# Optimization experiments

Measured on AMD Instinct MI355X. Metric: run time of the kernel, lower is better.

## Reference

```python
import jax, jax.numpy as jnp
import numpy as np

SEGMENT_LENGTHS = [1024, 2048, 4096]
DILATION_RATES = [1, 2, 4]


def _head_groups(num_heads, num_segments):
    base = num_heads // num_segments
    extra = num_heads % num_segments
    groups = [base] * num_segments
    for i in range(extra):
        groups[-(i + 1)] += 1
    return groups


def _dilated_indices(segment_len, dilation_rate, offset):
    # Mirrors RingDilatedAttentionV2._apply_dilation index construction (static).
    if dilation_rate > 1:
        idx = np.arange(offset, segment_len, dilation_rate)
        repeats = (segment_len + len(idx) - 1) // len(idx)
        idx = np.tile(idx, repeats)[:segment_len] % segment_len
    else:
        idx = np.arange(segment_len)
    return jnp.asarray(idx, dtype=jnp.int32)


def setup_inputs() -> dict:
    key = jax.random.key(0)
    kq, kk, kv = jax.random.split(key, 3)
    b, n, h, d = 1, 4096, 12, 64
    return {
        "query": jax.random.normal(kq, (b, n, h, d), dtype=jnp.float32),
        "key": jax.random.normal(kk, (b, n, h, d), dtype=jnp.float32),
        "value": jax.random.normal(kv, (b, n, h, d), dtype=jnp.float32),
        "is_causal": 1,
    }


def _dilated_attention(query, key, value, is_causal):
    b, n, h, d = query.shape
    groups = _head_groups(h, len(SEGMENT_LENGTHS))
    scale = 1.0 / np.sqrt(d).astype(np.float32)
    outs = []
    head_start = 0
    for i, (seg_len, rate, g) in enumerate(zip(SEGMENT_LENGTHS, DILATION_RATES, groups)):
        if g == 0:
            continue
        sl = min(seg_len, n)
        ns = n // sl  # n chosen divisible by every segment length
        q = query[:, :, head_start:head_start + g, :].reshape(b, ns, sl, g, d)
        k = key[:, :, head_start:head_start + g, :].reshape(b, ns, sl, g, d)
        v = value[:, :, head_start:head_start + g, :].reshape(b, ns, sl, g, d)
        if rate > 1 or i > 0:
            idx = _dilated_indices(sl, rate, i)
            k = k[:, :, idx]
            v = v[:, :, idx]
        # scores: [b, seg, heads, q_pos, k_pos]
        scores = jnp.einsum("bsqhd,bskhd->bshqk", q, k) * scale
        if is_causal:
            causal = jnp.triu(jnp.ones((sl, sl), dtype=bool), k=1)
            scores = jnp.where(causal, jnp.finfo(scores.dtype).min, scores)
        attn = jax.nn.softmax(scores, axis=-1)
        o = jnp.einsum("bshqk,bskhd->bsqhd", attn, v).reshape(b, n, g, d)
        outs.append(o)
        head_start += g
    return jnp.concatenate(outs, axis=2)  # [b, n, h, d]


def reference(query, key, value, is_causal):
    return _dilated_attention(query, key, value, is_causal)
```

## Files before the change

### kernel.cpp

```cpp
#include <hip/hip_runtime.h>
#include <hip/hip_bf16.h>
#include <math.h>

typedef __bf16 bf16x8 __attribute__((ext_vector_type(8)));
typedef float  f32x4  __attribute__((ext_vector_type(4)));
typedef float  f32x16 __attribute__((ext_vector_type(16)));
typedef unsigned int uint4v __attribute__((ext_vector_type(4)));
typedef unsigned short ushort_t;

#define LDK 72

#define KG_OFF  0
#define VGT_OFF 6291456
#define LACC_OFF 12582912

__device__ __forceinline__ int gather_pos(int gi, int group) {
    const int lsl = 10 + group;
    const int seg = gi >> lsl;
    const int j   = gi - (seg << lsl);
    return (seg << lsl) + group + ((j & 1023) << group);
}

__device__ __forceinline__ void gld_lds16(const ushort_t* g, __bf16* l) {
    __builtin_amdgcn_global_load_lds(
        (const __attribute__((address_space(1))) void*)g,
        (__attribute__((address_space(3))) void*)l, 16, 0, 0);
}

__device__ __forceinline__ unsigned int pk_bf16(float lo, float hi) {
    unsigned short a = __builtin_bit_cast(unsigned short, (__bf16)lo);
    unsigned short b = __builtin_bit_cast(unsigned short, (__bf16)hi);
    return ((unsigned int)b << 16) | (unsigned int)a;
}

__device__ __forceinline__ f32x16 zero16() {
    f32x16 z;
    #pragma unroll
    for (int i = 0; i < 16; ++i) z[i] = 0.f;
    return z;
}

__global__ __launch_bounds__(256)
void preconvert_kernel(const float* __restrict__ K, const float* __restrict__ V,
                       ushort_t* __restrict__ Kg, ushort_t* __restrict__ VgT)
{
    const int HD = 768;
    int b = blockIdx.x;
    const int tid = threadIdx.x;
    if (b < 768) {
        const int h = b % 12, gi0 = (b / 12) * 64;
        const int group = h >> 2;
        const int gi = gi0 + (tid >> 2);
        const int d0 = (tid & 3) << 4;
        const int pos = gather_pos(gi, group);
        const float* kp = K + (size_t)pos * HD + h * 64 + d0;
        float4 x0 = ((const float4*)kp)[0], x1 = ((const float4*)kp)[1];
        float4 x2 = ((const float4*)kp)[2], x3 = ((const float4*)kp)[3];
        bf16x8 w0, w1;
        w0[0]=(__bf16)x0.x; w0[1]=(__bf16)x0.y; w0[2]=(__bf16)x0.z; w0[3]=(__bf16)x0.w;
        w0[4]=(__bf16)x1.x; w0[5]=(__bf16)x1.y; w0[6]=(__bf16)x1.z; w0[7]=(__bf16)x1.w;
        w1[0]=(__bf16)x2.x; w1[1]=(__bf16)x2.y; w1[2]=(__bf16)x2.z; w1[3]=(__bf16)x2.w;
        w1[4]=(__bf16)x3.x; w1[5]=(__bf16)x3.y; w1[6]=(__bf16)x3.z; w1[7]=(__bf16)x3.w;
        ushort_t* out = Kg + ((size_t)(h * 4096 + gi)) * 64 + d0;
        *(bf16x8*)out = w0;
        *(bf16x8*)(out + 8) = w1;
    } else {
        b -= 768;
        const int h = b % 12, gi0 = (b / 12) * 64;
        const int group = h >> 2;
        __shared__ __align__(16) __bf16 Ts[64 * LDK];
        const int gil = tid >> 2;
        const int d0 = (tid & 3) << 4;
        const int pos = gather_pos(gi0 + gil, group);
        const float* vp = V + (size_t)pos * HD + h * 64 + d0;
        float4 x0 = ((const float4*)vp)[0], x1 = ((const float4*)vp)[1];
        float4 x2 = ((const float4*)vp)[2], x3 = ((const float4*)vp)[3];
        bf16x8 w0, w1;
        w0[0]=(__bf16)x0.x; w0[1]=(__bf16)x0.y; w0[2]=(__bf16)x0.z; w0[3]=(__bf16)x0.w;
        w0[4]=(__bf16)x1.x; w0[5]=(__bf16)x1.y; w0[6]=(__bf16)x1.z; w0[7]=(__bf16)x1.w;
        w1[0]=(__bf16)x2.x; w1[1]=(__bf16)x2.y; w1[2]=(__bf16)x2.z; w1[3]=(__bf16)x2.w;
        w1[4]=(__bf16)x3.x; w1[5]=(__bf16)x3.y; w1[6]=(__bf16)x3.z; w1[7]=(__bf16)x3.w;
        *(bf16x8*)&Ts[gil * LDK + d0]     = w0;
        *(bf16x8*)&Ts[gil * LDK + d0 + 8] = w1;
        __syncthreads();
        const int d = tid >> 2, c = tid & 3;
        bf16x8 o0, o1;
        #pragma unroll
        for (int i = 0; i < 8; ++i) {
            o0[i] = Ts[(c * 16 + i) * LDK + d];
            o1[i] = Ts[(c * 16 + 8 + i) * LDK + d];
        }
        ushort_t* out = VgT + ((size_t)(h * 64 + d)) * 4096 + gi0 + c * 16;
        *(bf16x8*)out = o0;
        *(bf16x8*)(out + 8) = o1;
    }
}

__global__ __launch_bounds__(256)
void dilated_attn_kernel(const float* __restrict__ Q,
                         const ushort_t* __restrict__ Kg,
                         const ushort_t* __restrict__ VgT,
                         const int* __restrict__ is_causal_p,
                         float* __restrict__ Out,
                         float* __restrict__ l_acc)
{
    const int HD = 768;
    const int bx  = blockIdx.x;
    const int qt  = 31 - (bx / 48);
    const int rem = bx % 48;
    const int h   = rem % 12;
    const int c   = rem / 12;
    const int group = h >> 2;
    const int sl    = 1024 << group;
    const int causal = (*is_causal_p) != 0;

    const int q0 = qt << 7;
    const int qb = q0 & (sl - 1);
    const int seg_start = q0 - qb;
    const int blk_diag = (qb + 127) >> 6;
    const int nkt = causal ? (blk_diag + 1) : (sl >> 6);
    const int kt0 = c << 4;
    if (kt0 >= nkt) return;
    const int kend = min(kt0 + 16, nkt);
    const int nch  = (nkt + 15) >> 4;

    const int tid  = threadIdx.x;
    const int wave = tid >> 6;
    const int lane = tid & 63;
    const int l31  = lane & 31;
    const int hi   = lane >> 5;

    __shared__ __align__(16) __bf16 Ks[2][64 * 64];
    __shared__ __align__(16) __bf16 Vs[2][64 * 64];

    const ushort_t* kg_head = Kg + (size_t)h * 4096 * 64;
    const ushort_t* vt_head = VgT + (size_t)h * 64 * 4096;

    const int bx16 = (((lane & 7) ^ (lane >> 3)) & 7) << 3;
    const int r8   = lane >> 3;

    auto stage = [&](int kt, int buf) {
        const ushort_t* kb = kg_head + ((size_t)(seg_start + (kt << 6)) << 6);
        const ushort_t* vb = vt_head + seg_start + (kt << 6);
        #pragma unroll
        for (int i = 0; i < 2; ++i) {
            const int row = i * 32 + wave * 8 + r8;
            gld_lds16(kb + row * 64 + bx16, &Ks[buf][(i * 32 + wave * 8) * 64]);
            gld_lds16(vb + (size_t)row * 4096 + bx16, &Vs[buf][(i * 32 + wave * 8) * 64]);
        }
    };

    const int qrow = q0 + wave * 32 + l31;
    const float* qptr = Q + (size_t)qrow * HD + h * 64;
    bf16x8 qf[4];
    {
        const float s = 0.125f * 1.4426950408889634f;
        #pragma unroll
        for (int ds = 0; ds < 4; ++ds) {
            float4 x0 = ((const float4*)(qptr + ds * 16 + hi * 8))[0];
            float4 x1 = ((const float4*)(qptr + ds * 16 + hi * 8))[1];
            bf16x8 w;
            w[0]=(__bf16)(x0.x*s); w[1]=(__bf16)(x0.y*s); w[2]=(__bf16)(x0.z*s); w[3]=(__bf16)(x0.w*s);
            w[4]=(__bf16)(x1.x*s); w[5]=(__bf16)(x1.y*s); w[6]=(__bf16)(x1.z*s); w[7]=(__bf16)(x1.w*s);
            qf[ds] = w;
        }
    }

    const int mydiag = causal ? ((qb + wave * 32 + 31) >> 6) : 0x7fffffff;
    const int lrow   = ((wave & 1) << 5) + l31;

    f32x16 o0 = zero16(), o1 = zero16();
    float l_part = 0.f;

    stage(kt0, 0);
    __syncthreads();

    for (int kt = kt0; kt < kend; ++kt) {
        const int cur = (kt - kt0) & 1;
        if (kt + 1 < kend) stage(kt + 1, cur ^ 1);

        if (kt <= mydiag) {
            f32x16 s0 = zero16(), s1 = zero16();
            const int xr = (l31 & 7);
            __builtin_amdgcn_s_setprio(1);
            #pragma unroll
            for (int ds = 0; ds < 4; ++ds) {
                const int cb = ds * 2 + hi;
                bf16x8 k0 = *(const bf16x8*)&Ks[cur][l31 * 64        + ((cb ^ xr) << 3)];
                bf16x8 k1 = *(const bf16x8*)&Ks[cur][(32 + l31) * 64 + ((cb ^ xr) << 3)];
                s0 = __builtin_amdgcn_mfma_f32_32x32x16_bf16(k0, qf[ds], s0, 0, 0, 0);
                s1 = __builtin_amdgcn_mfma_f32_32x32x16_bf16(k1, qf[ds], s1, 0, 0, 0);
            }
            __builtin_amdgcn_s_setprio(0);

            float p[2][16];
            const bool isdiag = causal && (kt == mydiag);
            #pragma unroll
            for (int r = 0; r < 16; ++r) {
                float v0 = exp2f(s0[r]);
                float v1 = exp2f(s1[r]);
                if (isdiag) {
                    const int kl = (r & 3) + ((r >> 2) << 3) + (hi << 2);
                    if (kl > lrow)      v0 = 0.f;
                    if (kl + 32 > lrow) v1 = 0.f;
                }
                p[0][r] = v0; p[1][r] = v1;
                l_part += v0 + v1;
            }

            __builtin_amdgcn_s_setprio(1);
            #pragma unroll
            for (int b = 0; b < 2; ++b) {
                #pragma unroll
                for (int ks2 = 0; ks2 < 2; ++ks2) {
                    const int g = ks2 * 8;
                    unsigned int x0 = pk_bf16(p[b][g + 0], p[b][g + 1]);
                    unsigned int x1 = pk_bf16(p[b][g + 2], p[b][g + 3]);
                    unsigned int y0 = pk_bf16(p[b][g + 4], p[b][g + 5]);
                    unsigned int y1 = pk_bf16(p[b][g + 6], p[b][g + 7]);
                    unsigned int sx0 = (unsigned int)__shfl_xor((int)x0, 32);
                    unsigned int sx1 = (unsigned int)__shfl_xor((int)x1, 32);
                    unsigned int sy0 = (unsigned int)__shfl_xor((int)y0, 32);
                    unsigned int sy1 = (unsigned int)__shfl_xor((int)y1, 32);
                    uint4v t;
                    t[0] = hi ? sy0 : x0;
                    t[1] = hi ? sy1 : x1;
                    t[2] = hi ? y0 : sx0;
                    t[3] = hi ? y1 : sx1;
                    bf16x8 pa = __builtin_bit_cast(bf16x8, t);
                    const int kcb = (b * 2 + ks2) * 2 + hi;
                    bf16x8 v0 = *(const bf16x8*)&Vs[cur][l31 * 64        + ((kcb ^ xr) << 3)];
                    bf16x8 v1 = *(const bf16x8*)&Vs[cur][(32 + l31) * 64 + ((kcb ^ xr) << 3)];
                    o0 = __builtin_amdgcn_mfma_f32_32x32x16_bf16(pa, v0, o0, 0, 0, 0);
                    o1 = __builtin_amdgcn_mfma_f32_32x32x16_bf16(pa, v1, o1, 0, 0, 0);
                }
            }
            __builtin_amdgcn_s_setprio(0);
        }

        __syncthreads();
    }

    const float l2 = l_part + __shfl_xor(l_part, 32);
    const int qw = q0 + wave * 32;
    if (nch == 1) {
        const float inv = 1.0f / l2;
        #pragma unroll
        for (int r = 0; r < 16; ++r) {
            const int qloc = (r & 3) + ((r >> 2) << 3) + (hi << 2);
            const float invq = __shfl(inv, qloc);
            const int row = qw + qloc;
            Out[(size_t)row * HD + h * 64 + l31]      = o0[r] * invq;
            Out[(size_t)row * HD + h * 64 + 32 + l31] = o1[r] * invq;
        }
    } else {
        if (hi == 0) atomicAdd(&l_acc[(qw + l31) * 12 + h], l2);
        #pragma unroll
        for (int r = 0; r < 16; ++r) {
            const int qloc = (r & 3) + ((r >> 2) << 3) + (hi << 2);
            const int row = qw + qloc;
            atomicAdd(&Out[(size_t)row * HD + h * 64 + l31],      o0[r]);
            atomicAdd(&Out[(size_t)row * HD + h * 64 + 32 + l31], o1[r]);
        }
    }
}

__global__ __launch_bounds__(256)
void finalize_kernel(float* __restrict__ Out, const float* __restrict__ l_acc,
                     const int* __restrict__ is_causal_p)
{
    const int causal = (*is_causal_p) != 0;
    const int idx = blockIdx.x * 256 + threadIdx.x;
    const int rh = idx >> 4;
    const int d4 = idx & 15;
    const int h = rh % 12;
    const int row = rh / 12;
    const int group = h >> 2;
    const int ntf = 16 << group;
    const int qt128 = row >> 7;
    const int qb_t = (qt128 << 1) & (ntf - 1);
    const int nkt = causal ? (qb_t + 2) : ntf;
    if (nkt <= 16) return;
    const float inv = 1.0f / l_acc[rh];
    float4* p = (float4*)Out + (size_t)rh * 16 + d4;
    float4 v = *p;
    v.x *= inv; v.y *= inv; v.z *= inv; v.w *= inv;
    *p = v;
}

extern "C" void kernel_launch(void* const* d_in, const int* in_sizes, int n_in,
                              void* d_out, int out_size, void* d_ws, size_t ws_size,
                              hipStream_t stream) {
    (void)in_sizes; (void)n_in; (void)out_size; (void)ws_size;
    const float* Q = (const float*)d_in[0];
    const float* K = (const float*)d_in[1];
    const float* V = (const float*)d_in[2];
    const int* isc = (const int*)d_in[3];
    float* Out = (float*)d_out;
    ushort_t* Kg   = (ushort_t*)((char*)d_ws + KG_OFF);
    ushort_t* VgT  = (ushort_t*)((char*)d_ws + VGT_OFF);
    float*    lacc = (float*)((char*)d_ws + LACC_OFF);

    hipMemsetAsync(Out, 0, (size_t)4096 * 12 * 64 * 4, stream);
    hipMemsetAsync(lacc, 0, (size_t)4096 * 12 * 4, stream);
    preconvert_kernel<<<1536, 256, 0, stream>>>(K, V, Kg, VgT);
    dilated_attn_kernel<<<1536, 256, 0, stream>>>(Q, Kg, VgT, isc, Out, lacc);
    finalize_kernel<<<3072, 256, 0, stream>>>(Out, lacc, isc);
}
```

Measured before the change: 148.7 us.

## Fold memsets into preconvert, restructure loop barriers, use permlane32 swap

Drops the two hipMemsetAsync calls and zeroes Out and l_acc inside the preconvert kernel, removing two launches. The attention loop now issues the first tile load before Q conversion and uses one vmcnt wait plus barrier at the top of each iteration instead of a trailing __syncthreads. The four shfl_xor calls plus selects in the P repack are replaced with two permlane32_swap instructions. The barrier change must still keep the double buffer from being overwritten before all waves finish reading it.

New measurement: 143.0 us. 1.04x faster.

```diff
diff --git a/kernel.cpp b/kernel.cpp
--- a/kernel.cpp
+++ b/kernel.cpp
@@ -5,6 +5,7 @@
 typedef __bf16 bf16x8 __attribute__((ext_vector_type(8)));
 typedef float  f32x4  __attribute__((ext_vector_type(4)));
 typedef float  f32x16 __attribute__((ext_vector_type(16)));
+typedef int    int2v  __attribute__((ext_vector_type(2)));
 typedef unsigned int uint4v __attribute__((ext_vector_type(4)));
 typedef unsigned short ushort_t;
 
@@ -42,12 +43,18 @@
 
 __global__ __launch_bounds__(256)
 void preconvert_kernel(const float* __restrict__ K, const float* __restrict__ V,
-                       ushort_t* __restrict__ Kg, ushort_t* __restrict__ VgT)
+                       ushort_t* __restrict__ Kg, ushort_t* __restrict__ VgT,
+                       float* __restrict__ Out, float* __restrict__ l_acc)
 {
     const int HD = 768;
     int b = blockIdx.x;
     const int tid = threadIdx.x;
     if (b < 768) {
+        {
+            float4 z = {0.f, 0.f, 0.f, 0.f};
+            float4* zp = (float4*)Out + ((size_t)b * 256 + tid) * 4;
+            zp[0] = z; zp[1] = z; zp[2] = z; zp[3] = z;
+        }
         const int h = b % 12, gi0 = (b / 12) * 64;
         const int group = h >> 2;
         const int gi = gi0 + (tid >> 2);
@@ -66,6 +73,7 @@
         *(bf16x8*)(out + 8) = w1;
     } else {
         b -= 768;
+        if (b < 192) l_acc[b * 256 + tid] = 0.f;
         const int h = b % 12, gi0 = (b / 12) * 64;
         const int group = h >> 2;
         __shared__ __align__(16) __bf16 Ts[64 * LDK];
@@ -150,6 +158,8 @@
         }
     };
 
+    stage(kt0, 0);
+
     const int qrow = q0 + wave * 32 + l31;
     const float* qptr = Q + (size_t)qrow * HD + h * 64;
     bf16x8 qf[4];
@@ -172,11 +182,13 @@
     f32x16 o0 = zero16(), o1 = zero16();
     float l_part = 0.f;
 
-    stage(kt0, 0);
-    __syncthreads();
-
     for (int kt = kt0; kt < kend; ++kt) {
         const int cur = (kt - kt0) & 1;
+
+        asm volatile("s_waitcnt vmcnt(0)" ::: "memory");
+        __builtin_amdgcn_s_barrier();
+        __builtin_amdgcn_sched_barrier(0);
+
         if (kt + 1 < kend) stage(kt + 1, cur ^ 1);
 
         if (kt <= mydiag) {
@@ -214,19 +226,17 @@
                 #pragma unroll
                 for (int ks2 = 0; ks2 < 2; ++ks2) {
                     const int g = ks2 * 8;
-                    unsigned int x0 = pk_bf16(p[b][g + 0], p[b][g + 1]);
-                    unsigned int x1 = pk_bf16(p[b][g + 2], p[b][g + 3]);
-                    unsigned int y0 = pk_bf16(p[b][g + 4], p[b][g + 5]);
-                    unsigned int y1 = pk_bf16(p[b][g + 6], p[b][g + 7]);
-                    unsigned int sx0 = (unsigned int)__shfl_xor((int)x0, 32);
-                    unsigned int sx1 = (unsigned int)__shfl_xor((int)x1, 32);
-                    unsigned int sy0 = (unsigned int)__shfl_xor((int)y0, 32);
-                    unsigned int sy1 = (unsigned int)__shfl_xor((int)y1, 32);
+                    int x0 = (int)pk_bf16(p[b][g + 0], p[b][g + 1]);
+                    int x1 = (int)pk_bf16(p[b][g + 2], p[b][g + 3]);
+                    int y0 = (int)pk_bf16(p[b][g + 4], p[b][g + 5]);
+                    int y1 = (int)pk_bf16(p[b][g + 6], p[b][g + 7]);
+                    int2v r02 = __builtin_amdgcn_permlane32_swap(x0, y0, false, false);
+                    int2v r13 = __builtin_amdgcn_permlane32_swap(x1, y1, false, false);
                     uint4v t;
-                    t[0] = hi ? sy0 : x0;
-                    t[1] = hi ? sy1 : x1;
-                    t[2] = hi ? y0 : sx0;
-                    t[3] = hi ? y1 : sx1;
+                    t[0] = (unsigned int)r02[0];
+                    t[1] = (unsigned int)r13[0];
+                    t[2] = (unsigned int)r02[1];
+                    t[3] = (unsigned int)r13[1];
                     bf16x8 pa = __builtin_bit_cast(bf16x8, t);
                     const int kcb = (b * 2 + ks2) * 2 + hi;
                     bf16x8 v0 = *(const bf16x8*)&Vs[cur][l31 * 64        + ((kcb ^ xr) << 3)];
@@ -237,8 +247,6 @@
             }
             __builtin_amdgcn_s_setprio(0);
         }
-
-        __syncthreads();
     }
 
     const float l2 = l_part + __shfl_xor(l_part, 32);
@@ -301,9 +309,7 @@
     ushort_t* VgT  = (ushort_t*)((char*)d_ws + VGT_OFF);
     float*    lacc = (float*)((char*)d_ws + LACC_OFF);
 
-    hipMemsetAsync(Out, 0, (size_t)4096 * 12 * 64 * 4, stream);
-    hipMemsetAsync(lacc, 0, (size_t)4096 * 12 * 4, stream);
-    preconvert_kernel<<<1536, 256, 0, stream>>>(K, V, Kg, VgT);
+    preconvert_kernel<<<1536, 256, 0, stream>>>(K, V, Kg, VgT, Out, lacc);
     dilated_attn_kernel<<<1536, 256, 0, stream>>>(Q, Kg, VgT, isc, Out, lacc);
     finalize_kernel<<<3072, 256, 0, stream>>>(Out, lacc, isc);
 }
```
